# Kernel optimization log

Hardware: AMD Instinct MI355X
Metric: run time of the kernel (lower is better)

The kernel has to match this reference:

```python
import jax, jax.numpy as jnp
import numpy as np

B, RES, DIM, H, KD = 16, 32, 768, 12, 64
N = RES * RES          # 1024 tokens
D = KD                 # attn_ratio = 1 -> per-head value dim == key_dim
DH = D * H             # 768
SCALE = KD ** -0.5
LN_EPS = 1e-5


def _bias_idxs():
    # replicate the itertools.product construction: for row-major points,
    # offsets (|dy|,|dx|) are first seen in order dy-major, so id = |dy|*RES + |dx|
    coords = np.arange(N)
    y, x = coords // RES, coords % RES
    dy = np.abs(y[:, None] - y[None, :])
    dx = np.abs(x[:, None] - x[None, :])
    return jnp.asarray(dy * RES + dx, dtype=jnp.int32)  # [N, N]


def setup_inputs() -> dict:
    key = jax.random.key(0)
    ks = jax.random.split(key, 8)
    return {
        "x": jax.random.normal(ks[0], (B, N, DIM), jnp.float32),
        "ln_w": 1.0 + 0.01 * jax.random.normal(ks[1], (DIM,), jnp.float32),
        "ln_b": 0.01 * jax.random.normal(ks[2], (DIM,), jnp.float32),
        "qkv_w": 0.02 * jax.random.normal(ks[3], (3 * H * KD, DIM), jnp.float32),
        "qkv_b": 0.01 * jax.random.normal(ks[4], (3 * H * KD,), jnp.float32),
        "proj_w": 0.02 * jax.random.normal(ks[5], (DIM, DH), jnp.float32),
        "proj_b": 0.01 * jax.random.normal(ks[6], (DIM,), jnp.float32),
        "attn_biases": 0.1 * jax.random.normal(ks[7], (H, RES * RES), jnp.float32),
        "bias_idxs": _bias_idxs(),
    }


def reference(x, ln_w, ln_b, qkv_w, qkv_b, proj_w, proj_b, attn_biases, bias_idxs):
    # LayerNorm over the feature dim
    mu = jnp.mean(x, axis=-1, keepdims=True)
    var = jnp.mean(jnp.square(x - mu), axis=-1, keepdims=True)
    xn = (x - mu) * jax.lax.rsqrt(var + LN_EPS) * ln_w + ln_b

    # fused qkv projection -> [B, N, H, 3*KD], split per head
    qkv = (xn @ qkv_w.T + qkv_b).reshape(B, N, H, 3 * KD)
    q, k, v = jnp.split(qkv, [KD, 2 * KD], axis=3)  # each [B, N, H, KD]

    # gathered relative-position bias: [H, N, N]
    bias = attn_biases[:, bias_idxs]

    # scores + bias -> softmax -> AV
    attn = jnp.einsum("bnhk,bmhk->bhnm", q, k) * SCALE + bias[None]
    attn = jax.nn.softmax(attn, axis=-1)
    out = jnp.einsum("bhnm,bmhd->bnhd", attn, v).reshape(B, N, DH)
    return out @ proj_w.T + proj_b
```

## Files before the change

### kernel.cpp

```cpp
#include <hip/hip_runtime.h>
#include <cstdint>
#include <cstddef>

#define AS1 __attribute__((address_space(1)))
#define AS3 __attribute__((address_space(3)))

typedef float f32x4 __attribute__((ext_vector_type(4)));
typedef __bf16 bf16x8 __attribute__((ext_vector_type(8)));
typedef __bf16 bf16x4 __attribute__((ext_vector_type(4)));
typedef uint32_t u32x4 __attribute__((ext_vector_type(4)));

__device__ __forceinline__ void async_cp16(void* lds, const void* g) {
    __builtin_amdgcn_global_load_lds((AS1 void*)(g), (AS3 void*)(lds), 16, 0, 0);
}

__device__ __forceinline__ bf16x8 frag_of(u32x4 u) {
    return __builtin_bit_cast(bf16x8, u);
}

__global__ __launch_bounds__(256)
void cvt_w(const float* __restrict__ qkvw, const float* __restrict__ projw,
           __bf16* __restrict__ qkvwb, __bf16* __restrict__ projwb) {
    int i = blockIdx.x * 256 + threadIdx.x;
    if (i < 442368) {
        int row = i / 192, c4 = (i - row * 192) * 4;
        int t = (row >= 1536) ? 2 : (row >= 768 ? 1 : 0);
        int rem = row - t * 768;
        int hh = rem >> 6, d = rem & 63;
        int in_row = hh * 192 + t * 64 + d;
        float4 v = *(const float4*)(qkvw + (long)in_row * 768 + c4);
        bf16x4 o;
        o[0] = (__bf16)v.x; o[1] = (__bf16)v.y; o[2] = (__bf16)v.z; o[3] = (__bf16)v.w;
        *(bf16x4*)(qkvwb + (long)row * 768 + c4) = o;
    } else {
        int j = i - 442368;
        float4 v = ((const float4*)projw)[j];
        bf16x4 o;
        o[0] = (__bf16)v.x; o[1] = (__bf16)v.y; o[2] = (__bf16)v.z; o[3] = (__bf16)v.w;
        ((bf16x4*)projwb)[j] = o;
    }
}

__global__ __launch_bounds__(256)
void ln_kernel(const float* __restrict__ x, const float* __restrict__ w,
               const float* __restrict__ bsh, __bf16* __restrict__ xn) {
    const int lane = threadIdx.x & 63;
    const long row = (long)blockIdx.x * 4 + (threadIdx.x >> 6);
    const float4* xr = (const float4*)(x + row * 768);
    float4 v[3];
    v[0] = xr[lane]; v[1] = xr[lane + 64]; v[2] = xr[lane + 128];
    float s = 0.f, ss = 0.f;
#pragma unroll
    for (int i = 0; i < 3; ++i) {
        s  += v[i].x + v[i].y + v[i].z + v[i].w;
        ss += v[i].x * v[i].x + v[i].y * v[i].y + v[i].z * v[i].z + v[i].w * v[i].w;
    }
#pragma unroll
    for (int m = 1; m < 64; m <<= 1) { s += __shfl_xor(s, m); ss += __shfl_xor(ss, m); }
    const float mean = s * (1.f / 768.f);
    const float rstd = rsqrtf(ss * (1.f / 768.f) - mean * mean + 1e-5f);
    const float4* wv = (const float4*)w;
    const float4* bv = (const float4*)bsh;
    bf16x4* outp = (bf16x4*)(xn + row * 768);
#pragma unroll
    for (int i = 0; i < 3; ++i) {
        float4 wi = wv[lane + 64 * i], bi = bv[lane + 64 * i];
        bf16x4 o;
        o[0] = (__bf16)((v[i].x - mean) * rstd * wi.x + bi.x);
        o[1] = (__bf16)((v[i].y - mean) * rstd * wi.y + bi.y);
        o[2] = (__bf16)((v[i].z - mean) * rstd * wi.z + bi.z);
        o[3] = (__bf16)((v[i].w - mean) * rstd * wi.w + bi.w);
        outp[lane + 64 * i] = o;
    }
}

template <int MODE>
__device__ __forceinline__
void gemm_core(char* smem,
               const __bf16* __restrict__ A, const __bf16* __restrict__ Bw,
               const float* __restrict__ bias,
               __bf16* __restrict__ q_out, __bf16* __restrict__ k_out,
               __bf16* __restrict__ vt_out, float* __restrict__ f_out,
               long bm, long bn) {
    constexpr int K = 768;
    const int tid  = threadIdx.x;
    const int lane = tid & 63;
    const int quad = lane >> 4;
    const int l16  = lane & 15;
    const int wave = tid >> 6;
    const int wm = wave >> 1, wn = wave & 1;

    const __bf16* Ab = A  + bm * K;
    const __bf16* Bb = Bw + bn * K;

    const int e0 = tid, e1 = tid + 256;
    const int rA0 = e0 >> 2, c0 = ((e0 & 3) ^ ((e0 >> 3) & 3)) * 8;
    const int rA1 = e1 >> 2, c1 = ((e1 & 3) ^ ((e1 >> 3) & 3)) * 8;
    const int swq = quad ^ ((l16 >> 1) & 3);

    f32x4 acc[4][4] = {};

    auto stage = [&](int t) {
        char* base = smem + (t % 3) * 16384;
        const __bf16* As_ = Ab + t * 32;
        const __bf16* Bs_ = Bb + t * 32;
        async_cp16(base + e0 * 16,        As_ + (long)rA0 * K + c0);
        async_cp16(base + e1 * 16,        As_ + (long)rA1 * K + c1);
        async_cp16(base + 8192 + e0 * 16, Bs_ + (long)rA0 * K + c0);
        async_cp16(base + 8192 + e1 * 16, Bs_ + (long)rA1 * K + c1);
    };

    auto kstep = [&](int buf) {
        const u32x4* Av = (const u32x4*)(smem + buf * 16384);
        const u32x4* Bv = (const u32x4*)(smem + buf * 16384 + 8192);
        bf16x8 af[4], bfr[4];
#pragma unroll
        for (int t = 0; t < 4; ++t) {
            af[t]  = frag_of(Av[(wm * 64 + t * 16 + l16) * 4 + swq]);
            bfr[t] = frag_of(Bv[(wn * 64 + t * 16 + l16) * 4 + swq]);
        }
        __builtin_amdgcn_s_setprio(1);
#pragma unroll
        for (int i = 0; i < 4; ++i)
#pragma unroll
            for (int j = 0; j < 4; ++j) {
                if constexpr (MODE == 0)
                    acc[i][j] = __builtin_amdgcn_mfma_f32_16x16x32_bf16(bfr[j], af[i], acc[i][j], 0, 0, 0);
                else
                    acc[i][j] = __builtin_amdgcn_mfma_f32_16x16x32_bf16(af[i], bfr[j], acc[i][j], 0, 0, 0);
            }
        __builtin_amdgcn_s_setprio(0);
    };

    stage(0); stage(1);
    for (int t = 0; t < 23; ++t) {
        asm volatile("s_waitcnt vmcnt(4)" ::: "memory");
        __builtin_amdgcn_s_barrier();
        if (t < 22) stage(t + 2);
        kstep(t % 3);
    }
    asm volatile("s_waitcnt vmcnt(0)" ::: "memory");
    __builtin_amdgcn_s_barrier();
    kstep(23 % 3);

    if constexpr (MODE == 0) {
#pragma unroll
        for (int j = 0; j < 4; ++j) {
            int col0 = (int)bn + wn * 64 + j * 16 + quad * 4;
            int t  = col0 >= 768;
            int cc = col0 - t * 768;
            int h  = cc >> 6, d = cc & 63;
            int f  = h * 192 + t * 64 + d;
            float4 bb = *(const float4*)(bias + f);
            __bf16* dst = t ? k_out : q_out;
#pragma unroll
            for (int i = 0; i < 4; ++i) {
                long row = bm + wm * 64 + i * 16 + l16;
                long b   = row >> 10;
                long n   = row & 1023;
                bf16x4 pk;
                pk[0] = (__bf16)(acc[i][j][0] + bb.x);
                pk[1] = (__bf16)(acc[i][j][1] + bb.y);
                pk[2] = (__bf16)(acc[i][j][2] + bb.z);
                pk[3] = (__bf16)(acc[i][j][3] + bb.w);
                *(bf16x4*)(dst + ((b * 12 + h) * 1024 + n) * 64 + d) = pk;
            }
        }
    } else if constexpr (MODE == 2) {
#pragma unroll
        for (int j = 0; j < 4; ++j) {
            int cv = (int)bn - 1536 + wn * 64 + j * 16 + l16;
            int h  = cv >> 6, d = cv & 63;
            float bv = bias[h * 192 + 128 + d];
#pragma unroll
            for (int i = 0; i < 4; ++i) {
                long row0 = bm + wm * 64 + i * 16 + quad * 4;
                long b    = row0 >> 10;
                long n0   = row0 & 1023;
                bf16x4 pk;
                pk[0] = (__bf16)(acc[i][j][0] + bv);
                pk[1] = (__bf16)(acc[i][j][1] + bv);
                pk[2] = (__bf16)(acc[i][j][2] + bv);
                pk[3] = (__bf16)(acc[i][j][3] + bv);
                *(bf16x4*)(vt_out + ((b * 12 + h) * 64 + d) * 1024 + n0) = pk;
            }
        }
    } else {
#pragma unroll
        for (int i = 0; i < 4; ++i) {
#pragma unroll
            for (int r = 0; r < 4; ++r) {
                long row = bm + wm * 64 + i * 16 + quad * 4 + r;
#pragma unroll
                for (int j = 0; j < 4; ++j) {
                    int col = (int)bn + wn * 64 + j * 16 + l16;
                    f_out[row * 768 + col] = acc[i][j][r] + bias[col];
                }
            }
        }
    }
}

__global__ __launch_bounds__(256, 3)
void gemm_qkv(const __bf16* __restrict__ A, const __bf16* __restrict__ Bw,
              const float* __restrict__ bias, __bf16* __restrict__ qb,
              __bf16* __restrict__ kb, __bf16* __restrict__ vtb) {
    __shared__ __align__(16) char smem[49152];
    int blk  = blockIdx.x;
    int xcd  = blk & 7;
    int rest = blk >> 3;
    int bx   = rest % 18;
    int byg  = rest / 18;
    long by  = xcd + 8 * byg;
    if (bx < 12)
        gemm_core<0>(smem, A, Bw, bias, qb, kb, nullptr, nullptr, by * 128, (long)bx * 128);
    else
        gemm_core<2>(smem, A, Bw, bias, nullptr, nullptr, vtb, nullptr, by * 128, (long)bx * 128);
}

__global__ __launch_bounds__(256, 3)
void gemm_proj(const __bf16* __restrict__ A, const __bf16* __restrict__ Bw,
               const float* __restrict__ bias, float* __restrict__ out) {
    __shared__ __align__(16) char smem[49152];
    int blk  = blockIdx.x;
    int xcd  = blk & 7;
    int rest = blk >> 3;
    int bx   = rest % 6;
    int byg  = rest / 6;
    long by  = xcd + 8 * byg;
    gemm_core<1>(smem, A, Bw, bias, nullptr, nullptr, nullptr, out,
                 by * 128, (long)bx * 128);
}

__global__ __launch_bounds__(256, 4)
void attn_kernel(const __bf16* __restrict__ Q, const __bf16* __restrict__ Kb,
                 const __bf16* __restrict__ Vt, const float* __restrict__ biases,
                 __bf16* __restrict__ out) {
    __shared__ __align__(16) char smem[28672];
    float* brow = (float*)(smem + 24576);

    const int tid  = threadIdx.x;
    const int lane = tid & 63;
    const int wave = tid >> 6;
    const int quad = lane >> 4;
    const int l16  = lane & 15;
    const int sw   = l16 & 7;
    const int swp  = (l16 >> 1) & 3;

    int blk  = blockIdx.x;
    int xcd  = blk & 7;
    int rest = blk >> 3;
    int qt   = rest & 7;
    int bhg  = rest >> 3;
    int bh_i = xcd + 8 * bhg;
    int b    = bh_i / 12;
    int h    = bh_i - b * 12;

    const long bh = bh_i;
    const __bf16* Qg  = Q  + (bh * 1024 + qt * 128) * 64;
    const __bf16* Kg  = Kb + bh * 1024 * 64;
    const __bf16* Vtg = Vt + bh * 64 * 1024;

    const int rk = tid >> 3;
    const int ck = (tid & 7) ^ (rk & 7);
    const int rv = tid >> 2;
    const int cv = (tid & 3) ^ ((tid >> 3) & 3);

    {
        const float LOG2E = 1.4426950408889634f;
        float4 v = ((const float4*)(biases + (long)h * 1024))[tid];
        float4 o; o.x = v.x * LOG2E; o.y = v.y * LOG2E;
        o.z = v.z * LOG2E; o.w = v.w * LOG2E;
        ((float4*)brow)[tid] = o;
    }
#pragma unroll
    for (int j = 0; j < 4; ++j) {
        int e = tid + 256 * j;
        int r = e >> 3, c = (e & 7) ^ (r & 7);
        async_cp16(smem + e * 16, Qg + r * 64 + c * 8);
    }
    __syncthreads();

    bf16x8 aq[2][2];
    {
        const u32x4* Qv = (const u32x4*)smem;
#pragma unroll
        for (int g = 0; g < 2; ++g) {
            int qrow = wave * 32 + g * 16 + l16;
            aq[g][0] = frag_of(Qv[qrow * 8 + (quad ^ sw)]);
            aq[g][1] = frag_of(Qv[qrow * 8 + ((quad + 4) ^ sw)]);
        }
    }
    __syncthreads();
    async_cp16(smem + tid * 16,        Kg  + rk * 64   + ck * 8);
    async_cp16(smem + 8192 + tid * 16, Vtg + rv * 1024 + cv * 8);
    __syncthreads();

    const int yq = 4 * qt + wave;
    int pdx00[4], pdx01[4], pdx10[4];
#pragma unroll
    for (int r = 0; r < 4; ++r) {
        int d0 = l16 - (quad * 4 + r);
        pdx00[r] = d0 < 0 ? -d0 : d0;
        pdx01[r] = 16 - d0;
        pdx10[r] = 16 + d0;
    }

    const float SSCALE = 0.125f * 1.4426950408889634f;
    float lacc[2] = {0.f, 0.f};
    f32x4 o[2][4] = {};
    char* Pw = smem + 16384 + wave * 2048;
    const int hb = (quad & 1) * 8;
    const int pslotw = (quad >> 1);

    for (int kt = 0; kt < 32; ++kt) {
        const int cb = kt & 1;
        if (kt < 31) {
            const int nb = cb ^ 1;
            async_cp16(smem + nb * 4096 + tid * 16,
                       Kg + (kt + 1) * 2048 + rk * 64 + ck * 8);
            async_cp16(smem + 8192 + nb * 4096 + tid * 16,
                       Vtg + (kt + 1) * 32 + rv * 1024 + cv * 8);
        }

        f32x4 s[2][2];
        const u32x4* Kv = (const u32x4*)(smem + cb * 4096);
#pragma unroll
        for (int nt = 0; nt < 2; ++nt) {
            int krow = nt * 16 + l16;
            bf16x8 k0 = frag_of(Kv[krow * 8 + (quad ^ sw)]);
            bf16x8 k1 = frag_of(Kv[krow * 8 + ((quad + 4) ^ sw)]);
#pragma unroll
            for (int g = 0; g < 2; ++g) {
                f32x4 z = {0.f, 0.f, 0.f, 0.f};
                z = __builtin_amdgcn_mfma_f32_16x16x32_bf16(k0, aq[g][0], z, 0, 0, 0);
                z = __builtin_amdgcn_mfma_f32_16x16x32_bf16(k1, aq[g][1], z, 0, 0, 0);
                s[g][nt] = z;
            }
        }

        int dyv = yq - kt; dyv = dyv < 0 ? -dyv : dyv;
        const float* br = brow + dyv * 32;
#pragma unroll
        for (int g = 0; g < 2; ++g) {
#pragma unroll
            for (int nt = 0; nt < 2; ++nt) {
                const int* pdx = (g == nt) ? pdx00 : (g ? pdx10 : pdx01);
                bf16x4 pk;
#pragma unroll
                for (int r = 0; r < 4; ++r) {
                    float p = __builtin_amdgcn_exp2f(s[g][nt][r] * SSCALE + br[pdx[r]]);
                    lacc[g] += p;
                    pk[r] = (__bf16)p;
                }
                int slot = (nt * 2 + pslotw) ^ swp;
                *(bf16x4*)(Pw + (g * 16 + l16) * 64 + slot * 16 + hb) = pk;
            }
        }

        bf16x8 bp[2];
#pragma unroll
        for (int g = 0; g < 2; ++g)
            bp[g] = frag_of(*(const u32x4*)(Pw + (g * 16 + l16) * 64 + ((quad ^ swp) << 4)));
        const char* Vb = smem + 8192 + cb * 4096;
#pragma unroll
        for (int dt = 0; dt < 4; ++dt) {
            bf16x8 vf = frag_of(*(const u32x4*)(Vb + (dt * 16 + l16) * 64 + ((quad ^ swp) << 4)));
#pragma unroll
            for (int g = 0; g < 2; ++g)
                o[g][dt] = __builtin_amdgcn_mfma_f32_16x16x32_bf16(vf, bp[g], o[g][dt], 0, 0, 0);
        }

        __syncthreads();
    }

#pragma unroll
    for (int g = 0; g < 2; ++g) {
        float la = lacc[g];
        la += __shfl_xor(la, 16);
        la += __shfl_xor(la, 32);
        const float rl = 1.f / la;
        const long n = qt * 128 + wave * 32 + g * 16 + l16;
        __bf16* op = out + ((long)b * 1024 + n) * 768 + h * 64 + quad * 4;
#pragma unroll
        for (int dt = 0; dt < 4; ++dt) {
            bf16x4 ov;
            ov[0] = (__bf16)(o[g][dt][0] * rl);
            ov[1] = (__bf16)(o[g][dt][1] * rl);
            ov[2] = (__bf16)(o[g][dt][2] * rl);
            ov[3] = (__bf16)(o[g][dt][3] * rl);
            *(bf16x4*)(op + dt * 16) = ov;
        }
    }
}

extern "C" void kernel_launch(void* const* d_in, const int* in_sizes, int n_in,
                              void* d_out, int out_size, void* d_ws, size_t ws_size,
                              hipStream_t stream) {
    (void)in_sizes; (void)n_in; (void)out_size; (void)ws_size;
    const float* x      = (const float*)d_in[0];
    const float* ln_w   = (const float*)d_in[1];
    const float* ln_b   = (const float*)d_in[2];
    const float* qkv_w  = (const float*)d_in[3];
    const float* qkv_b  = (const float*)d_in[4];
    const float* proj_w = (const float*)d_in[5];
    const float* proj_b = (const float*)d_in[6];
    const float* ab     = (const float*)d_in[7];
    float* outp = (float*)d_out;

    char* ws = (char*)d_ws;
    __bf16* xn     = (__bf16*)(ws);
    __bf16* aout   = (__bf16*)(ws);
    __bf16* qkvwb  = (__bf16*)(ws + 25165824);
    __bf16* projwb = (__bf16*)(ws + 28704768);
    __bf16* qb     = (__bf16*)(ws + 29884416);
    __bf16* kb     = (__bf16*)(ws + 55050240);
    __bf16* vtb    = (__bf16*)(ws + 80216064);

    cvt_w<<<2304, 256, 0, stream>>>(qkv_w, proj_w, qkvwb, projwb);
    ln_kernel<<<4096, 256, 0, stream>>>(x, ln_w, ln_b, xn);
    gemm_qkv<<<2304, 256, 0, stream>>>(xn, qkvwb, qkv_b, qb, kb, vtb);
    attn_kernel<<<1536, 256, 0, stream>>>(qb, kb, vtb, ab, aout);
    gemm_proj<<<768, 256, 0, stream>>>(aout, projwb, proj_b, outp);
}
```

Measured before the change: 298.7 us.

## Load GEMM weight fragments directly to registers, staging only A through LDS

After: 365.9 us. +22.5%, slower.

```diff
diff --git a/kernel.cpp b/kernel.cpp
--- a/kernel.cpp
+++ b/kernel.cpp
@@ -94,54 +94,76 @@
     const __bf16* Bb = Bw + bn * K;
 
     const int e0 = tid, e1 = tid + 256;
-    const int rA0 = e0 >> 2, c0 = ((e0 & 3) ^ ((e0 >> 3) & 3)) * 8;
-    const int rA1 = e1 >> 2, c1 = ((e1 & 3) ^ ((e1 >> 3) & 3)) * 8;
+    const int rA0 = e0 >> 2, cA0 = ((e0 & 3) ^ ((e0 >> 3) & 3)) * 8;
+    const int rA1 = e1 >> 2, cA1 = ((e1 & 3) ^ ((e1 >> 3) & 3)) * 8;
     const int swq = quad ^ ((l16 >> 1) & 3);
 
     f32x4 acc[4][4] = {};
 
-    auto stage = [&](int t) {
-        char* base = smem + (t % 3) * 16384;
-        const __bf16* As_ = Ab + t * 32;
-        const __bf16* Bs_ = Bb + t * 32;
-        async_cp16(base + e0 * 16,        As_ + (long)rA0 * K + c0);
-        async_cp16(base + e1 * 16,        As_ + (long)rA1 * K + c1);
-        async_cp16(base + 8192 + e0 * 16, Bs_ + (long)rA0 * K + c0);
-        async_cp16(base + 8192 + e1 * 16, Bs_ + (long)rA1 * K + c1);
+    const __bf16* bp0 = Bb + (long)(wn * 64 +  0 + l16) * K + quad * 8;
+    const __bf16* bp1 = Bb + (long)(wn * 64 + 16 + l16) * K + quad * 8;
+    const __bf16* bp2 = Bb + (long)(wn * 64 + 32 + l16) * K + quad * 8;
+    const __bf16* bp3 = Bb + (long)(wn * 64 + 48 + l16) * K + quad * 8;
+    u32x4 bsA[4], bsB[4];
+
+    const __bf16* Asrc = Ab;
+    char* sstage = smem;
+    char* sread  = smem;
+
+    auto stageA = [&]() {
+        async_cp16(sstage + e0 * 16, Asrc + (long)rA0 * K + cA0);
+        async_cp16(sstage + e1 * 16, Asrc + (long)rA1 * K + cA1);
+        Asrc += 32;
+        sstage += 8192; if (sstage == smem + 24576) sstage = smem;
     };
 
-    auto kstep = [&](int buf) {
-        const u32x4* Av = (const u32x4*)(smem + buf * 16384);
-        const u32x4* Bv = (const u32x4*)(smem + buf * 16384 + 8192);
-        bf16x8 af[4], bfr[4];
-#pragma unroll
-        for (int t = 0; t < 4; ++t) {
-            af[t]  = frag_of(Av[(wm * 64 + t * 16 + l16) * 4 + swq]);
-            bfr[t] = frag_of(Bv[(wn * 64 + t * 16 + l16) * 4 + swq]);
-        }
+    auto kstep = [&](u32x4 (&bs)[4]) {
+        const u32x4* Av = (const u32x4*)sread;
+        bf16x8 af[4];
+#pragma unroll
+        for (int t = 0; t < 4; ++t)
+            af[t] = frag_of(Av[(wm * 64 + t * 16 + l16) * 4 + swq]);
         __builtin_amdgcn_s_setprio(1);
 #pragma unroll
         for (int i = 0; i < 4; ++i)
 #pragma unroll
             for (int j = 0; j < 4; ++j) {
                 if constexpr (MODE == 0)
-                    acc[i][j] = __builtin_amdgcn_mfma_f32_16x16x32_bf16(bfr[j], af[i], acc[i][j], 0, 0, 0);
+                    acc[i][j] = __builtin_amdgcn_mfma_f32_16x16x32_bf16(frag_of(bs[j]), af[i], acc[i][j], 0, 0, 0);
                 else
-                    acc[i][j] = __builtin_amdgcn_mfma_f32_16x16x32_bf16(af[i], bfr[j], acc[i][j], 0, 0, 0);
+                    acc[i][j] = __builtin_amdgcn_mfma_f32_16x16x32_bf16(af[i], frag_of(bs[j]), acc[i][j], 0, 0, 0);
             }
         __builtin_amdgcn_s_setprio(0);
+        sread += 8192; if (sread == smem + 24576) sread = smem;
     };
 
-    stage(0); stage(1);
-    for (int t = 0; t < 23; ++t) {
-        asm volatile("s_waitcnt vmcnt(4)" ::: "memory");
+    auto bload = [&](u32x4 (&bs)[4]) {
+        asm volatile("global_load_dwordx4 %0, %1, off" : "=v"(bs[0]) : "v"(bp0) : "memory");
+        asm volatile("global_load_dwordx4 %0, %1, off" : "=v"(bs[1]) : "v"(bp1) : "memory");
+        asm volatile("global_load_dwordx4 %0, %1, off" : "=v"(bs[2]) : "v"(bp2) : "memory");
+        asm volatile("global_load_dwordx4 %0, %1, off" : "=v"(bs[3]) : "v"(bp3) : "memory");
+        bp0 += 32; bp1 += 32; bp2 += 32; bp3 += 32;
+    };
+
+    stageA(); bload(bsA);
+    stageA(); bload(bsB);
+
+    for (int t2 = 0; t2 < 12; ++t2) {
+        asm volatile("s_waitcnt vmcnt(6)" ::: "memory");
+        __builtin_amdgcn_sched_barrier(0);
         __builtin_amdgcn_s_barrier();
-        if (t < 22) stage(t + 2);
-        kstep(t % 3);
-    }
-    asm volatile("s_waitcnt vmcnt(0)" ::: "memory");
-    __builtin_amdgcn_s_barrier();
-    kstep(23 % 3);
+        if (t2 < 11) stageA();
+        kstep(bsA);
+        if (t2 < 11) bload(bsA);
+
+        if (t2 < 11) { asm volatile("s_waitcnt vmcnt(6)" ::: "memory"); }
+        else         { asm volatile("s_waitcnt vmcnt(0)" ::: "memory"); }
+        __builtin_amdgcn_sched_barrier(0);
+        __builtin_amdgcn_s_barrier();
+        if (t2 < 11) stageA();
+        kstep(bsB);
+        if (t2 < 11) bload(bsB);
+    }
 
     if constexpr (MODE == 0) {
 #pragma unroll
@@ -205,7 +227,7 @@
 void gemm_qkv(const __bf16* __restrict__ A, const __bf16* __restrict__ Bw,
               const float* __restrict__ bias, __bf16* __restrict__ qb,
               __bf16* __restrict__ kb, __bf16* __restrict__ vtb) {
-    __shared__ __align__(16) char smem[49152];
+    __shared__ __align__(16) char smem[24576];
     int blk  = blockIdx.x;
     int xcd  = blk & 7;
     int rest = blk >> 3;
@@ -221,7 +243,7 @@
 __global__ __launch_bounds__(256, 3)
 void gemm_proj(const __bf16* __restrict__ A, const __bf16* __restrict__ Bw,
                const float* __restrict__ bias, float* __restrict__ out) {
-    __shared__ __align__(16) char smem[49152];
+    __shared__ __align__(16) char smem[24576];
     int blk  = blockIdx.x;
     int xcd  = blk & 7;
     int rest = blk >> 3;
```
